# Kernel tuning notes

Hardware: AMD Instinct MI355X
Metric: run time of the kernel (lower is better)

The kernel has to match this reference:

```python
import jax, jax.numpy as jnp
import numpy as np

C = 256
CQK = C // 8


def setup_inputs() -> dict:
    key = jax.random.key(0)
    ks = jax.random.split(key, 8)
    B, H, W = 4, 64, 64
    inputs = jax.random.normal(ks[0], (B, H, W, C), dtype=jnp.float32)
    s = 1.0 / np.sqrt(C)
    Wq = jax.random.normal(ks[1], (C, CQK), dtype=jnp.float32) * s
    bq = jnp.zeros((CQK,), dtype=jnp.float32)
    Wk = jax.random.normal(ks[2], (C, CQK), dtype=jnp.float32) * s
    bk = jnp.zeros((CQK,), dtype=jnp.float32)
    Wv = jax.random.normal(ks[3], (C, C), dtype=jnp.float32) * s
    bv = jnp.zeros((C,), dtype=jnp.float32)
    gamma = jnp.float32(0.7)  # nonzero so attention branch contributes
    return {"inputs": inputs, "Wq": Wq, "bq": bq, "Wk": Wk, "bk": bk,
            "Wv": Wv, "bv": bv, "gamma": gamma}


def reference(inputs, Wq, bq, Wk, bk, Wv, bv, gamma):
    B, H, W, Cin = inputs.shape
    N = H * W
    x = inputs.reshape(B, N, Cin)
    # 1x1 convs == per-pixel channel matmuls
    q = x @ Wq + bq                      # (B, N, C//8)
    k = x @ Wk + bk                      # (B, N, C//8)
    v = x @ Wv + bv                      # (B, N, C)
    energy = jnp.einsum('bnd,bmd->bnm', q, k)   # (B, N, N), no scale (faithful)
    attn = jax.nn.softmax(energy, axis=-1)
    x_out = jnp.einsum('bnm,bmc->bnc', attn, v)  # (B, N, C)
    out = gamma * x_out.reshape(B, H, W, Cin) + inputs
    return out
```

## Files before the change

kernel.cpp:

```cpp
#include <hip/hip_runtime.h>
#include <hip/hip_bf16.h>

#define B_ 4
#define N_ 4096
#define C_ 256
#define D_ 32
#define LOG2E 1.44269504088896340736f
#define MFMA16 __builtin_amdgcn_mfma_f32_16x16x32_bf16

typedef __attribute__((ext_vector_type(8))) short short8;
typedef __attribute__((ext_vector_type(4))) short short4v;
typedef __attribute__((ext_vector_type(4))) float float4v;

__device__ inline short f2bf_rne(float f) {
  unsigned u = __builtin_bit_cast(unsigned, f);
  u += 0x7FFFu + ((u >> 16) & 1u);
  return (short)(u >> 16);
}
__device__ inline float bf2f(short s) {
  unsigned u = ((unsigned)(unsigned short)s) << 16;
  return __builtin_bit_cast(float, u);
}
__device__ inline float fast_exp2(float x) { return __builtin_amdgcn_exp2f(x); }

__device__ inline short4v pk4_bf16(float p0, float p1, float p2, float p3) {
  union { unsigned u[2]; short4v s; } r;
  asm("v_cvt_pk_bf16_f32 %0, %1, %2" : "=v"(r.u[0]) : "v"(p0), "v"(p1));
  asm("v_cvt_pk_bf16_f32 %0, %1, %2" : "=v"(r.u[1]) : "v"(p2), "v"(p3));
  return r.s;
}

__global__ __launch_bounds__(256) void cast_w_kernel(
    const float* __restrict__ Wq, const float* __restrict__ Wk,
    const float* __restrict__ Wv, short* __restrict__ WtF) {
  int i  = blockIdx.x * 256 + threadIdx.x;
  int j  = i & 7;
  int l  = (i >> 3) & 63;
  int ks = (i >> 9) & 7;
  int nb = i >> 12;
  int n  = nb * 16 + (l & 15);
  int k  = ks * 32 + ((l >> 4) << 3) + j;
  float v;
  if (n < 32)      v = Wq[k * 32 + n] * LOG2E;
  else if (n < 64) v = Wk[k * 32 + (n - 32)];
  else             v = Wv[k * 256 + (n - 64)];
  WtF[i] = f2bf_rne(v);
}

__global__ __launch_bounds__(256, 2) void proj_kernel(
    const float* __restrict__ x, const short* __restrict__ WtF,
    const float* __restrict__ bq, const float* __restrict__ bk,
    const float* __restrict__ bv,
    short* __restrict__ qb, short* __restrict__ kF, short* __restrict__ vF) {
  int blk = blockIdx.x;
  int b  = blk >> 7;
  int r0 = (blk & 127) * 32;
  int t  = threadIdx.x;
  int w  = t >> 6;
  int l  = t & 63;
  int lc = l & 15;
  int q4 = l >> 4;

  __shared__ __align__(16) short sA[32][272];
  __shared__ __align__(16) short sV[256][40];
  __shared__ __align__(16) short sK[32][36];

  {
    const float* xb = x + (size_t)(b * N_ + r0) * C_;
#pragma unroll
    for (int ch = 0; ch < 8; ch++) {
      int f   = ch * 256 + t;
      int row = f >> 6;
      int col = (f & 63) * 4;
      float4v v = *(const float4v*)(xb + f * 4);
      short4v s = pk4_bf16(v[0], v[1], v[2], v[3]);
      *(short4v*)(&sA[row][col]) = s;
    }
  }
  __syncthreads();

  float4v acc[10];
#pragma unroll
  for (int i = 0; i < 10; i++) { acc[i][0] = 0.f; acc[i][1] = 0.f; acc[i][2] = 0.f; acc[i][3] = 0.f; }

  const short* wbase = WtF + w * 4096 + l * 8;

#define LOADW(B0, B1, B2, B3, B4, KS)                       \
  B0 = *(const short8*)(wbase + (KS) * 512 + 0 * 16384);    \
  B1 = *(const short8*)(wbase + (KS) * 512 + 1 * 16384);    \
  B2 = *(const short8*)(wbase + (KS) * 512 + 2 * 16384);    \
  B3 = *(const short8*)(wbase + (KS) * 512 + 3 * 16384);    \
  B4 = *(const short8*)(wbase + (KS) * 512 + 4 * 16384);

#define DO_MFMA(A0, A1, B0, B1, B2, B3, B4)                 \
  acc[0] = MFMA16(A0, B0, acc[0], 0, 0, 0);                 \
  acc[1] = MFMA16(A1, B0, acc[1], 0, 0, 0);                 \
  acc[2] = MFMA16(A0, B1, acc[2], 0, 0, 0);                 \
  acc[3] = MFMA16(A1, B1, acc[3], 0, 0, 0);                 \
  acc[4] = MFMA16(A0, B2, acc[4], 0, 0, 0);                 \
  acc[5] = MFMA16(A1, B2, acc[5], 0, 0, 0);                 \
  acc[6] = MFMA16(A0, B3, acc[6], 0, 0, 0);                 \
  acc[7] = MFMA16(A1, B3, acc[7], 0, 0, 0);                 \
  acc[8] = MFMA16(A0, B4, acc[8], 0, 0, 0);                 \
  acc[9] = MFMA16(A1, B4, acc[9], 0, 0, 0);

  short8 wA0, wA1, wA2, wA3, wA4, wB0, wB1, wB2, wB3, wB4;
  LOADW(wA0, wA1, wA2, wA3, wA4, 0)
#pragma unroll
  for (int kk = 0; kk < 8; kk += 2) {
    short8 a00 = *(const short8*)(&sA[lc][kk * 32 + q4 * 8]);
    short8 a01 = *(const short8*)(&sA[16 + lc][kk * 32 + q4 * 8]);
    LOADW(wB0, wB1, wB2, wB3, wB4, kk + 1)
    DO_MFMA(a00, a01, wA0, wA1, wA2, wA3, wA4)
    short8 a10 = *(const short8*)(&sA[lc][(kk + 1) * 32 + q4 * 8]);
    short8 a11 = *(const short8*)(&sA[16 + lc][(kk + 1) * 32 + q4 * 8]);
    LOADW(wA0, wA1, wA2, wA3, wA4, kk + 2)
    DO_MFMA(a10, a11, wB0, wB1, wB2, wB3, wB4)
  }
#undef LOADW
#undef DO_MFMA

  {
    float bias0 = (w < 2) ? bq[w * 16 + lc] * LOG2E : bk[(w - 2) * 16 + lc];
#pragma unroll
    for (int rt = 0; rt < 2; rt++) {
      if (w < 2) {
#pragma unroll
        for (int r = 0; r < 4; r++) {
          int row = rt * 16 + q4 * 4 + r;
          qb[(size_t)(b * N_ + r0 + row) * D_ + w * 16 + lc] =
              f2bf_rne(acc[rt][r] + bias0);
        }
      } else {
#pragma unroll
        for (int r = 0; r < 4; r++) {
          int row = rt * 16 + q4 * 4 + r;
          sK[row][(w - 2) * 16 + lc] = f2bf_rne(acc[rt][r] + bias0);
        }
      }
    }
#pragma unroll
    for (int nbo = 1; nbo < 5; nbo++) {
      float bias = bv[(nbo - 1) * 64 + w * 16 + lc];
#pragma unroll
      for (int rt = 0; rt < 2; rt++) {
        float4v a = acc[nbo * 2 + rt];
        short4v pk = pk4_bf16(a[0] + bias, a[1] + bias, a[2] + bias, a[3] + bias);
        *(short4v*)(&sV[(nbo - 1) * 64 + w * 16 + lc][rt * 16 + q4 * 4]) = pk;
      }
    }
  }
  __syncthreads();

  int kt  = r0 >> 6;
  int ks0 = (r0 >> 5) & 1;

  {
    size_t tb2 = ((size_t)(b * 64 + kt) * 32 + ks0 * 16) * 512;
    int cb = t >> 4;
#pragma unroll
    for (int k = 0; k < 4; k++) {
      int p = (t & 15) * 4 + k;
      int j = p >> 4, i = p & 15;
      short8 vv = *(const short8*)(&sV[cb * 16 + i][j * 8]);
      *(short8*)(vF + tb2 + (size_t)t * 32 + k * 8) = vv;
    }
  }
  if (t < 128) {
    int fr = t >> 6, ll = t & 63;
    int kv = fr * 16 + (ll & 15), dg = ll >> 4;
    size_t tbk = ((size_t)(b * 64 + kt) * 4 + ks0 * 2) * 512;
    short8 kv8 = *(const short8*)(&sK[kv][dg * 8]);
    *(short8*)(kF + tbk + (size_t)t * 8) = kv8;
  }
}

__device__ __forceinline__ void barrier_lds_only() {
  asm volatile("s_waitcnt lgkmcnt(0)\n\ts_barrier" ::: "memory");
}

__global__ __launch_bounds__(512, 4) void flash_partial_kernel(
    const short* __restrict__ qb, const short* __restrict__ kF,
    const short* __restrict__ vF, short* __restrict__ obuf,
    float* __restrict__ lbuf) {
  int blk = blockIdx.x;
  int b  = blk & 3;
  int hb = (blk >> 2) & 1;
  int qt = blk >> 3;
  int r0 = qt * 64;
  int t  = threadIdx.x;
  int w  = t >> 6;
  int l  = t & 63;
  int lc = l & 15;
  int q4 = l >> 4;
  int rq = w & 3;
  int kh = w >> 2;

  __shared__ __align__(16) short sPn[2][4096];
  __shared__ float sL[4][16];

  int p = (b * 64 + qt) * 2 + hb;

  short8 qf = *(const short8*)(qb + (size_t)(b * N_ + r0 + rq * 16 + lc) * D_ + q4 * 8);

  const short* kbp = kF + ((size_t)(b * 64 + hb * 32) * 4) * 512 + kh * 1024 + l * 8;
  const short* vbp = vF + ((size_t)(b * 64 + hb * 32) * 32 + 2 * w) * 512 + l * 8;

  short8 kC0, kC1;
  short8 vX00, vX01, vX10, vX11;
  short8 vY00, vY01, vY10, vY11;

  kC0 = *(const short8*)(kbp + 0);
  kC1 = *(const short8*)(kbp + 512);
  vX00 = *(const short8*)(vbp + 0);
  vX01 = *(const short8*)(vbp + 512);
  vX10 = *(const short8*)(vbp + 8192);
  vX11 = *(const short8*)(vbp + 8704);

  float4v O[8];
#pragma unroll
  for (int i = 0; i < 8; i++) { O[i][0] = 0.f; O[i][1] = 0.f; O[i][2] = 0.f; O[i][3] = 0.f; }
  float l_part = 0.f;

  int qkbase = (rq * 2) * 512 + (((q4 >> 1) * 16) + lc) * 8 + (q4 & 1) * 4;

#define K_RELOAD(TI)                                                           \
  { size_t o_ = (size_t)(TI) * 2048;                                           \
    kC0 = *(const short8*)(kbp + o_);                                          \
    kC1 = *(const short8*)(kbp + o_ + 512); }

#define QK_STEP(SPB, VALID)                                                    \
  { __builtin_amdgcn_s_setprio(1);                                             \
    float4v z; z[0] = 0.f; z[1] = 0.f; z[2] = 0.f; z[3] = 0.f;                 \
    float4v S0 = MFMA16(kC0, qf, z, 0, 0, 0);                                  \
    float4v S1 = MFMA16(kC1, qf, z, 0, 0, 0);                                  \
    short* rowp = &sPn[SPB][qkbase + kh * 512];                                \
    float ts = 0.f;                                                            \
    { float p0 = fast_exp2(S0[0]), p1 = fast_exp2(S0[1]);                      \
      float p2 = fast_exp2(S0[2]), p3 = fast_exp2(S0[3]);                      \
      ts += (p0 + p1) + (p2 + p3);                                             \
      *(short4v*)(rowp + 0) = pk4_bf16(p0, p1, p2, p3); }                      \
    { float p0 = fast_exp2(S1[0]), p1 = fast_exp2(S1[1]);                      \
      float p2 = fast_exp2(S1[2]), p3 = fast_exp2(S1[3]);                      \
      ts += (p0 + p1) + (p2 + p3);                                             \
      *(short4v*)(rowp + 256) = pk4_bf16(p0, p1, p2, p3); }                    \
    __builtin_amdgcn_s_setprio(0);                                             \
    if (VALID) l_part += ts; }

#define PV_STEP(SPB, V00, V01, V10, V11)                                       \
  { _Pragma("unroll")                                                          \
    for (int rt = 0; rt < 4; rt++) {                                           \
      short8 pf0 = *(const short8*)(&sPn[SPB][(rt * 2 + 0) * 512 + l * 8]);    \
      short8 pf1 = *(const short8*)(&sPn[SPB][(rt * 2 + 1) * 512 + l * 8]);    \
      O[rt * 2 + 0] = MFMA16(pf0, V00, O[rt * 2 + 0], 0, 0, 0);                \
      O[rt * 2 + 0] = MFMA16(pf1, V10, O[rt * 2 + 0], 0, 0, 0);                \
      O[rt * 2 + 1] = MFMA16(pf0, V01, O[rt * 2 + 1], 0, 0, 0);                \
      O[rt * 2 + 1] = MFMA16(pf1, V11, O[rt * 2 + 1], 0, 0, 0);                \
    } }

  QK_STEP(0, true)
  K_RELOAD(1)
  barrier_lds_only();

  for (int ti = 0; ti < 32; ti += 2) {
    int n1 = ti + 1;
    int n2 = (ti + 2 < 32) ? ti + 2 : 31;
    bool v2 = (ti + 2 < 32);
    int n3 = (ti + 3 < 32) ? ti + 3 : 31;

    { size_t vo = (size_t)n1 * 16384;
      vY00 = *(const short8*)(vbp + vo);
      vY01 = *(const short8*)(vbp + vo + 512);
      vY10 = *(const short8*)(vbp + vo + 8192);
      vY11 = *(const short8*)(vbp + vo + 8704); }
    QK_STEP(1, true)
    K_RELOAD(n2)
    PV_STEP(0, vX00, vX01, vX10, vX11)
    barrier_lds_only();

    { size_t vo = (size_t)n2 * 16384;
      vX00 = *(const short8*)(vbp + vo);
      vX01 = *(const short8*)(vbp + vo + 512);
      vX10 = *(const short8*)(vbp + vo + 8192);
      vX11 = *(const short8*)(vbp + vo + 8704); }
    QK_STEP(0, v2)
    K_RELOAD(n3)
    PV_STEP(1, vY00, vY01, vY10, vY11)
    barrier_lds_only();
  }
#undef K_RELOAD
#undef QK_STEP
#undef PV_STEP

  {
    short* ob = obuf + ((size_t)p * 64 + w * 8) * 256 + l * 4;
#pragma unroll
    for (int a = 0; a < 8; a++) {
      float4v o = O[a];
      *(short4v*)(ob + a * 256) = pk4_bf16(o[0], o[1], o[2], o[3]);
    }
  }
  {
    float l_tot = l_part + __shfl_xor(l_part, 16, 64);
    l_tot += __shfl_xor(l_tot, 32, 64);
    if (kh == 0 && q4 == 0) sL[rq][lc] = l_tot;
    __syncthreads();
    if (kh == 1 && q4 == 0)
      lbuf[(size_t)p * 64 + rq * 16 + lc] = l_tot + sL[rq][lc];
  }
}

__global__ __launch_bounds__(256) void merge_kernel(
    const short* __restrict__ obuf, const float* __restrict__ lbuf,
    const float* __restrict__ xin, const float* __restrict__ gptr,
    float* __restrict__ out) {
  int blk2 = blockIdx.x;
  int blk  = blk2 >> 1;
  int h    = blk2 & 1;
  int t    = threadIdx.x;
  float g  = *gptr;

  __shared__ float sS[32][260];
  __shared__ float sGLinv[32];

  const short* o0 = obuf + (size_t)(blk * 2 + 0) * 16384;
  const short* o1 = obuf + (size_t)(blk * 2 + 1) * 16384;
  const float* l0 = lbuf + (size_t)(blk * 2 + 0) * 64;
  const float* l1 = lbuf + (size_t)(blk * 2 + 1) * 64;
  size_t gbase = (size_t)blk * 16384;

  if (t < 32)
    sGLinv[t] = g * __builtin_amdgcn_rcpf(l0[32 * h + t] + l1[32 * h + t]);

#pragma unroll
  for (int j = 0; j < 4; j++) {
    int gdx    = j * 256 + t;
    int chunk  = gdx >> 7;
    int within = gdx & 127;
    int offs   = (chunk * 8 + 4 * h) * 256 + within * 8;
    short8 a8 = *(const short8*)(o0 + offs);
    short8 c8 = *(const short8*)(o1 + offs);
    int s_in  = within >> 5;
    int pos8  = within & 31;
    int rt    = 2 * h + (s_in >> 1);
    int cbo   = s_in & 1;
    int chB   = chunk * 32 + cbo * 16;
#pragma unroll
    for (int e = 0; e < 8; e++) {
      int lane = pos8 * 2 + (e >> 2);
      int r    = e & 3;
      int row  = (rt & 1) * 16 + (lane >> 4) * 4 + r;
      int ch   = chB + (lane & 15);
      sS[row][ch] = bf2f(a8[e]) + bf2f(c8[e]);
    }
  }
  __syncthreads();

#pragma unroll
  for (int j = 0; j < 8; j++) {
    int gdx = j * 1024 + t * 4;
    int row = gdx >> 8;
    int ch  = gdx & 255;
    float gl = sGLinv[row];
    size_t gi = gbase + (size_t)(32 * h) * 256 + gdx;
    float4v xv = *(const float4v*)(xin + gi);
    float4v sv = *(const float4v*)(&sS[row][ch]);
    float4v ov;
#pragma unroll
    for (int e = 0; e < 4; e++) ov[e] = sv[e] * gl + xv[e];
    *(float4v*)(out + gi) = ov;
  }
}

extern "C" void kernel_launch(void* const* d_in, const int* in_sizes, int n_in,
                              void* d_out, int out_size, void* d_ws, size_t ws_size,
                              hipStream_t stream) {
  const float* x     = (const float*)d_in[0];
  const float* Wq    = (const float*)d_in[1];
  const float* bq    = (const float*)d_in[2];
  const float* Wk    = (const float*)d_in[3];
  const float* bk    = (const float*)d_in[4];
  const float* Wv    = (const float*)d_in[5];
  const float* bv    = (const float*)d_in[6];
  const float* gamma = (const float*)d_in[7];
  float* out = (float*)d_out;

  char* ws = (char*)d_ws;
  short* qb   = (short*)ws;
  short* kF   = (short*)(ws + (1u << 20));
  short* vF   = (short*)(ws + (2u << 20));
  short* WtF  = (short*)(ws + (10u << 20));
  short* obuf = (short*)(ws + (11u << 20));
  float* lbuf = (float*)(ws + (28u << 20));

  hipLaunchKernelGGL(cast_w_kernel,        dim3(320), dim3(256), 0, stream, Wq, Wk, Wv, WtF);
  hipLaunchKernelGGL(proj_kernel,          dim3(512), dim3(256), 0, stream, x, WtF, bq, bk, bv, qb, kF, vF);
  hipLaunchKernelGGL(flash_partial_kernel, dim3(512), dim3(512), 0, stream, qb, kF, vF, obuf, lbuf);
  hipLaunchKernelGGL(merge_kernel,         dim3(512), dim3(256), 0, stream, obuf, lbuf, x, gamma, out);
}
```

Baseline: 136.8 us.

## Drop KV split and fuse merge epilogue into flash attention kernel

```diff
diff --git a/kernel.cpp b/kernel.cpp
--- a/kernel.cpp
+++ b/kernel.cpp
@@ -179,14 +179,13 @@
   asm volatile("s_waitcnt lgkmcnt(0)\n\ts_barrier" ::: "memory");
 }
 
-__global__ __launch_bounds__(512, 4) void flash_partial_kernel(
+__global__ __launch_bounds__(512, 4) void flash_fused_kernel(
     const short* __restrict__ qb, const short* __restrict__ kF,
-    const short* __restrict__ vF, short* __restrict__ obuf,
-    float* __restrict__ lbuf) {
+    const short* __restrict__ vF, const float* __restrict__ xin,
+    const float* __restrict__ gptr, float* __restrict__ out) {
   int blk = blockIdx.x;
   int b  = blk & 3;
-  int hb = (blk >> 2) & 1;
-  int qt = blk >> 3;
+  int qt = blk >> 2;
   int r0 = qt * 64;
   int t  = threadIdx.x;
   int w  = t >> 6;
@@ -198,13 +197,14 @@
 
   __shared__ __align__(16) short sPn[2][4096];
   __shared__ float sL[4][16];
-
-  int p = (b * 64 + qt) * 2 + hb;
+  __shared__ float sLinv[64];
+
+  float g = *gptr;
 
   short8 qf = *(const short8*)(qb + (size_t)(b * N_ + r0 + rq * 16 + lc) * D_ + q4 * 8);
 
-  const short* kbp = kF + ((size_t)(b * 64 + hb * 32) * 4) * 512 + kh * 1024 + l * 8;
-  const short* vbp = vF + ((size_t)(b * 64 + hb * 32) * 32 + 2 * w) * 512 + l * 8;
+  const short* kbp = kF + ((size_t)(b * 64) * 4) * 512 + kh * 1024 + l * 8;
+  const short* vbp = vF + ((size_t)(b * 64) * 32 + 2 * w) * 512 + l * 8;
 
   short8 kC0, kC1;
   short8 vX00, vX01, vX10, vX11;
@@ -262,11 +262,11 @@
   K_RELOAD(1)
   barrier_lds_only();
 
-  for (int ti = 0; ti < 32; ti += 2) {
+  for (int ti = 0; ti < 64; ti += 2) {
     int n1 = ti + 1;
-    int n2 = (ti + 2 < 32) ? ti + 2 : 31;
-    bool v2 = (ti + 2 < 32);
-    int n3 = (ti + 3 < 32) ? ti + 3 : 31;
+    int n2 = (ti + 2 < 64) ? ti + 2 : 63;
+    bool v2 = (ti + 2 < 64);
+    int n3 = (ti + 3 < 64) ? ti + 3 : 63;
 
     { size_t vo = (size_t)n1 * 16384;
       vY00 = *(const short8*)(vbp + vo);
@@ -293,82 +293,31 @@
 #undef PV_STEP
 
   {
-    short* ob = obuf + ((size_t)p * 64 + w * 8) * 256 + l * 4;
-#pragma unroll
-    for (int a = 0; a < 8; a++) {
-      float4v o = O[a];
-      *(short4v*)(ob + a * 256) = pk4_bf16(o[0], o[1], o[2], o[3]);
-    }
-  }
-  {
     float l_tot = l_part + __shfl_xor(l_part, 16, 64);
     l_tot += __shfl_xor(l_tot, 32, 64);
     if (kh == 0 && q4 == 0) sL[rq][lc] = l_tot;
     __syncthreads();
     if (kh == 1 && q4 == 0)
-      lbuf[(size_t)p * 64 + rq * 16 + lc] = l_tot + sL[rq][lc];
-  }
-}
-
-__global__ __launch_bounds__(256) void merge_kernel(
-    const short* __restrict__ obuf, const float* __restrict__ lbuf,
-    const float* __restrict__ xin, const float* __restrict__ gptr,
-    float* __restrict__ out) {
-  int blk2 = blockIdx.x;
-  int blk  = blk2 >> 1;
-  int h    = blk2 & 1;
-  int t    = threadIdx.x;
-  float g  = *gptr;
-
-  __shared__ float sS[32][260];
-  __shared__ float sGLinv[32];
-
-  const short* o0 = obuf + (size_t)(blk * 2 + 0) * 16384;
-  const short* o1 = obuf + (size_t)(blk * 2 + 1) * 16384;
-  const float* l0 = lbuf + (size_t)(blk * 2 + 0) * 64;
-  const float* l1 = lbuf + (size_t)(blk * 2 + 1) * 64;
-  size_t gbase = (size_t)blk * 16384;
-
-  if (t < 32)
-    sGLinv[t] = g * __builtin_amdgcn_rcpf(l0[32 * h + t] + l1[32 * h + t]);
-
-#pragma unroll
-  for (int j = 0; j < 4; j++) {
-    int gdx    = j * 256 + t;
-    int chunk  = gdx >> 7;
-    int within = gdx & 127;
-    int offs   = (chunk * 8 + 4 * h) * 256 + within * 8;
-    short8 a8 = *(const short8*)(o0 + offs);
-    short8 c8 = *(const short8*)(o1 + offs);
-    int s_in  = within >> 5;
-    int pos8  = within & 31;
-    int rt    = 2 * h + (s_in >> 1);
-    int cbo   = s_in & 1;
-    int chB   = chunk * 32 + cbo * 16;
-#pragma unroll
-    for (int e = 0; e < 8; e++) {
-      int lane = pos8 * 2 + (e >> 2);
-      int r    = e & 3;
-      int row  = (rt & 1) * 16 + (lane >> 4) * 4 + r;
-      int ch   = chB + (lane & 15);
-      sS[row][ch] = bf2f(a8[e]) + bf2f(c8[e]);
-    }
-  }
-  __syncthreads();
-
-#pragma unroll
-  for (int j = 0; j < 8; j++) {
-    int gdx = j * 1024 + t * 4;
-    int row = gdx >> 8;
-    int ch  = gdx & 255;
-    float gl = sGLinv[row];
-    size_t gi = gbase + (size_t)(32 * h) * 256 + gdx;
-    float4v xv = *(const float4v*)(xin + gi);
-    float4v sv = *(const float4v*)(&sS[row][ch]);
-    float4v ov;
-#pragma unroll
-    for (int e = 0; e < 4; e++) ov[e] = sv[e] * gl + xv[e];
-    *(float4v*)(out + gi) = ov;
+      sLinv[rq * 16 + lc] = g * __builtin_amdgcn_rcpf(l_tot + sL[rq][lc]);
+    __syncthreads();
+  }
+
+  {
+#pragma unroll
+    for (int a = 0; a < 8; a++) {
+      int rt   = a >> 1;
+      int cbo  = a & 1;
+      int row0 = rt * 16 + q4 * 4;
+      int chg  = w * 32 + cbo * 16 + lc;
+      size_t gi = (size_t)(b * N_ + r0 + row0) * C_ + chg;
+      const float* xp = xin + gi;
+      float* op = out + gi;
+      float4v o = O[a];
+#pragma unroll
+      for (int r = 0; r < 4; r++) {
+        op[(size_t)r * C_] = o[r] * sLinv[row0 + r] + xp[(size_t)r * C_];
+      }
+    }
   }
 }
 
@@ -390,11 +339,8 @@
   short* kF   = (short*)(ws + (1u << 20));
   short* vF   = (short*)(ws + (2u << 20));
   short* WtF  = (short*)(ws + (10u << 20));
-  short* obuf = (short*)(ws + (11u << 20));
-  float* lbuf = (float*)(ws + (28u << 20));
-
-  hipLaunchKernelGGL(cast_w_kernel,        dim3(320), dim3(256), 0, stream, Wq, Wk, Wv, WtF);
-  hipLaunchKernelGGL(proj_kernel,          dim3(512), dim3(256), 0, stream, x, WtF, bq, bk, bv, qb, kF, vF);
-  hipLaunchKernelGGL(flash_partial_kernel, dim3(512), dim3(512), 0, stream, qb, kF, vF, obuf, lbuf);
-  hipLaunchKernelGGL(merge_kernel,         dim3(512), dim3(256), 0, stream, obuf, lbuf, x, gamma, out);
-}
+
+  hipLaunchKernelGGL(cast_w_kernel,      dim3(320), dim3(256), 0, stream, Wq, Wk, Wv, WtF);
+  hipLaunchKernelGGL(proj_kernel,        dim3(512), dim3(256), 0, stream, x, WtF, bq, bk, bv, qb, kF, vF);
+  hipLaunchKernelGGL(flash_fused_kernel, dim3(256), dim3(512), 0, stream, qb, kF, vF, x, gamma, out);
+}
```

After: 132.2 us (median of 2 runs). -3.3%, faster.
